# Performance work log

Measured on AMD Instinct MI355X. Metric: run time of the kernel, lower is better.

Reference implementation:

```python
import jax, jax.numpy as jnp
import numpy as np

MEMORY_SIZE = 512
PATTERN_DIM = 256
NUM_WAVELENGTHS = 3
ATTENTION_FOCUS = 1.0
CORRELATION_THRESHOLD = 0.3
H_NOISE = 0.03  # noise scale for the holographic medium buffer


def setup_inputs() -> dict:
    key = jax.random.key(0)
    k1, k2, k3 = jax.random.split(key, 3)
    B, R = 32, 128  # batch, rows per stimulus (R * PATTERN_DIM flat features)
    stimulus = jax.random.normal(k1, (B, R * PATTERN_DIM), dtype=jnp.float32)
    H_real = jax.random.normal(k2, (MEMORY_SIZE, PATTERN_DIM, NUM_WAVELENGTHS), dtype=jnp.float32) * H_NOISE
    H_imag = jax.random.normal(k3, (MEMORY_SIZE, PATTERN_DIM, NUM_WAVELENGTHS), dtype=jnp.float32) * H_NOISE
    return {"stimulus": stimulus, "H_real": H_real, "H_imag": H_imag}


def reference(stimulus, H_real, H_imag):
    # Faithful 'retrieve' mode of HolographicAssociativeMemory, fully vectorized.
    B = stimulus.shape[0]
    q = stimulus.reshape(B, -1, PATTERN_DIM).astype(jnp.complex64)  # [B, R, P]
    qf = jnp.fft.fft2(q, axes=(-2, -1))                             # [B, R, P]
    R = qf.shape[1]

    # query_fft[b, mem_idx % R] for every memory slot -> gather rows
    rows = jnp.arange(MEMORY_SIZE) % R
    q_rows = qf[:, rows, :]                                         # [B, M, P]

    H = (H_real + 1j * H_imag).astype(jnp.complex64)                # [M, P, W]
    phases = jnp.linspace(0.0, 2.0 * np.pi, NUM_WAVELENGTHS).astype(jnp.float32)
    ref_beams = jnp.exp(1j * phases).astype(jnp.complex64)          # [W]

    # reconstruction = query_fft_row * stored_hologram * reference_beam
    recon = q_rows[:, :, :, None] * H[None, :, :, :] * ref_beams    # [B, M, P, W]
    # torch.fft.ifft2 on a (1, P) tensor == ifft along P (size-1 axis is identity)
    rec = jnp.fft.ifft(recon, axis=2)                               # [B, M, P, W]
    corr = jnp.abs(rec).mean(axis=2)                                # [B, M, W]
    avg_corr = corr.mean(axis=-1)                                   # [B, M]

    focused = avg_corr * jnp.float32(ATTENTION_FOCUS)
    retrieved = jnp.where(focused > jnp.float32(CORRELATION_THRESHOLD), focused, jnp.float32(0.0))
    return retrieved
```

## Files before the change

### kernel.cpp

```cpp
#include <hip/hip_runtime.h>
#include <math.h>


#define TWO_PI 6.28318530717958647692f
#define PI_F   3.14159265358979323846f

#if __has_builtin(__builtin_amdgcn_permlane16_swap)
#define USE_PL16 1
#else
#define USE_PL16 0
#endif
#if __has_builtin(__builtin_amdgcn_permlane32_swap)
#define USE_PL32 1
#else
#define USE_PL32 0
#endif

typedef float f2 __attribute__((ext_vector_type(2)));
typedef unsigned int uint2v __attribute__((ext_vector_type(2)));

__device__ inline f2 mkf2(float x, float y) { f2 r; r[0] = x; r[1] = y; return r; }
__device__ inline f2 conjf2(f2 a) { return mkf2(a[0], -a[1]); }

__device__ inline f2 cmul(f2 a, f2 b) {
    const f2 axx = __builtin_shufflevector(a, a, 0, 0);
    const f2 ayn = mkf2(-a[1], a[1]);
    const f2 byx = __builtin_shufflevector(b, b, 1, 0);
    return axx * b + ayn * byx;
}
__device__ inline f2 csq(f2 a) { return cmul(a, a); }
__device__ inline f2 ab2(f2 A, f2 v, f2 B, f2 o) {
    const f2 Axx = __builtin_shufflevector(A, A, 0, 0);
    const f2 Ayn = mkf2(-A[1], A[1]);
    const f2 Bxx = __builtin_shufflevector(B, B, 0, 0);
    const f2 Byn = mkf2(-B[1], B[1]);
    const f2 vyx = __builtin_shufflevector(v, v, 1, 0);
    const f2 oyx = __builtin_shufflevector(o, o, 1, 0);
    return Axx * v + Ayn * vyx + Bxx * o + Byn * oyx;
}
__device__ inline f2 cfma2(f2 S, f2 b, f2 a) {
    const f2 Sxx = __builtin_shufflevector(S, S, 0, 0);
    const f2 Syn = mkf2(-S[1], S[1]);
    const f2 byx = __builtin_shufflevector(b, b, 1, 0);
    return Sxx * b + (Syn * byx + a);
}
__device__ inline f2 shfl_xor_c(f2 v, int mask) {
    return mkf2(__shfl_xor(v[0], mask, 64), __shfl_xor(v[1], mask, 64));
}

#define DPP_XOR1 0xB1
#define DPP_XOR2 0x4E
template <int CTRL>
__device__ inline f2 dpp_quad(f2 v) {
    return mkf2(
        __int_as_float(__builtin_amdgcn_update_dpp(__float_as_int(v[0]), __float_as_int(v[0]),
                                                   CTRL, 0xF, 0xF, false)),
        __int_as_float(__builtin_amdgcn_update_dpp(__float_as_int(v[1]), __float_as_int(v[1]),
                                                   CTRL, 0xF, 0xF, false)));
}

#if USE_PL16
__device__ inline void swap16c(f2 v, f2& a, f2& b) {
    uint2v rx = __builtin_amdgcn_permlane16_swap(__float_as_uint(v[0]), __float_as_uint(v[0]), false, false);
    uint2v ry = __builtin_amdgcn_permlane16_swap(__float_as_uint(v[1]), __float_as_uint(v[1]), false, false);
    a = mkf2(__uint_as_float(rx[0]), __uint_as_float(ry[0]));
    b = mkf2(__uint_as_float(rx[1]), __uint_as_float(ry[1]));
}
#endif
#if USE_PL32
__device__ inline void swap32c(f2 v, f2& a, f2& b) {
    uint2v rx = __builtin_amdgcn_permlane32_swap(__float_as_uint(v[0]), __float_as_uint(v[0]), false, false);
    uint2v ry = __builtin_amdgcn_permlane32_swap(__float_as_uint(v[1]), __float_as_uint(v[1]), false, false);
    a = mkf2(__uint_as_float(rx[0]), __uint_as_float(ry[0]));
    b = mkf2(__uint_as_float(rx[1]), __uint_as_float(ry[1]));
}
#endif

__global__ __launch_bounds__(256) void k_cols(const float* __restrict__ x,
                                              f2* __restrict__ yc,
                                              const float* __restrict__ Hr,
                                              const float* __restrict__ Hi,
                                              f2* __restrict__ Ht) {
    if (blockIdx.x >= 512) {
        const int idx = (blockIdx.x - 512) * 256 + threadIdx.x;
        const int m = idx / 768;
        const int rem = idx - m * 768;
        const int w = rem >> 8;
        const int p = rem & 255;
        const int k = __brev((unsigned)p) >> 24;
        const int src = (m * 256 + k) * 3 + w;
        Ht[idx] = mkf2(Hr[src], Hi[src]);
        return;
    }

    __shared__ f2 sm[128][17];
    __shared__ f2 tw[64];
    const int tid = threadIdx.x;

    if (tid < 64) {
        float sn, cs;
        __sincosf(-TWO_PI * (float)tid * (1.0f / 128.0f), &sn, &cs);
        tw[tid] = mkf2(cs, sn);
    }

    const int b  = blockIdx.x >> 4;
    const int d0 = (blockIdx.x & 15) << 4;
    const int c  = tid & 15;
    const int r0 = tid >> 4;
    const size_t base = (size_t)b * 32768 + (size_t)d0 + (size_t)c;

#pragma unroll
    for (int r = r0; r < 128; r += 16) {
        sm[__brev((unsigned)r) >> 25][c] = mkf2(x[base + (size_t)r * 256], 0.0f);
    }
    __syncthreads();

#pragma unroll
    for (int st = 0; st < 7; ++st) {
        const int half = 1 << st;
#pragma unroll
        for (int k = 0; k < 4; ++k) {
            const int idx = tid + (k << 8);
            const int cc  = idx & 15;
            const int j   = idx >> 4;
            const int pos = j & (half - 1);
            const int i0  = (j << 1) - pos;
            const int i1  = i0 + half;
            const f2 w  = tw[pos << (6 - st)];
            const f2 a  = sm[i0][cc];
            const f2 bv = cmul(sm[i1][cc], w);
            sm[i0][cc] = a + bv;
            sm[i1][cc] = a - bv;
        }
        __syncthreads();
    }

#pragma unroll
    for (int r = r0; r < 128; r += 16) {
        yc[base + (size_t)r * 256] = sm[r][c];
    }
}

__global__ __launch_bounds__(256) void k_recon(const f2* __restrict__ yc,
                                               const f2* __restrict__ Ht,
                                               float* __restrict__ out) {
    __shared__ f2 sh[256];
    const int lane = threadIdx.x & 63;
    const int wid  = threadIdx.x >> 6;
    const int b    = blockIdx.x >> 7;
    const int r    = blockIdx.x & 127;
    const int m    = r + (wid << 7);

    float sn, cs;
    __sincosf(PI_F * (float)lane * (1.0f / 128.0f), &sn, &cs);
    const f2 wi0 = mkf2(cs, sn);
    const f2 w64 = csq(wi0);
    const f2 S32 = csq(w64);
    const f2 S16 = csq(S32);
    const f2 b16 = csq(S16);
    const f2 b32 = csq(b16);
    const f2 b64 = csq(b32);
    const f2 one = mkf2(1.0f, 0.0f);
    const f2 A8 = (lane & 8) ? b16 : one, B8 = (lane & 8) ? one : b16;
    const f2 A4 = (lane & 4) ? b32 : one, B4 = (lane & 4) ? one : b32;
    const f2 A2 = (lane & 2) ? b64 : one, B2 = (lane & 2) ? one : b64;
    const f2 sg1 = (lane & 1) ? mkf2(-1.0f, -1.0f) : mkf2(1.0f, 1.0f);
    const f2 wi1 = mkf2(-wi0[1], wi0[0]);
#if !USE_PL16
    const f2 A16 = (lane & 16) ? S16 : one, B16 = (lane & 16) ? one : S16;
#endif
#if !USE_PL32
    const f2 A32 = (lane & 32) ? S32 : one, B32 = (lane & 32) ? one : S32;
#endif

    {
        const f2 gam    = conjf2(wi0);
        const f2 w128_0 = gam;
        const f2 w128_1 = mkf2(gam[1], -gam[0]);
        const f2 w64f = conjf2(w64);
        const f2 g4   = conjf2(S32);
        const f2 g8   = conjf2(S16);
        const f2 g16  = conjf2(b16);
        const f2 g32  = conjf2(b32);
        const f2 g64  = conjf2(b64);
#if USE_PL32
        const f2 P32 = (lane & 32) ? mkf2(-g4[0], -g4[1]) : one;
        const f2 Q32 = (lane & 32) ? g4 : one;
#else
        const f2 A32f = (lane & 32) ? g4 : one;
        const f2 B32f = (lane & 32) ? mkf2(-g4[0], -g4[1]) : one;
#endif
#if USE_PL16
        const f2 P16 = (lane & 16) ? mkf2(-g8[0], -g8[1]) : one;
        const f2 Q16 = (lane & 16) ? g8 : one;
#else
        const f2 A16f = (lane & 16) ? g8 : one;
        const f2 B16f = (lane & 16) ? mkf2(-g8[0], -g8[1]) : one;
#endif
        const f2 A8f = (lane & 8) ? g16 : one;
        const f2 B8f = (lane & 8) ? mkf2(-g16[0], -g16[1]) : one;
        const f2 A4f = (lane & 4) ? g32 : one;
        const f2 B4f = (lane & 4) ? mkf2(-g32[0], -g32[1]) : one;
        const f2 A2f = (lane & 2) ? g64 : one;
        const f2 B2f = (lane & 2) ? mkf2(-g64[0], -g64[1]) : one;

        const f2* xr = yc + ((size_t)(b * 128 + r)) * 256;
        f2 v0 = xr[lane];
        f2 v1 = xr[64 + lane];
        f2 v2 = xr[128 + lane];
        f2 v3 = xr[192 + lane];

        { f2 a = v0; v0 = a + v2; v2 = cmul(a - v2, w128_0); }
        { f2 a = v1; v1 = a + v3; v3 = cmul(a - v3, w128_1); }
        { f2 a = v0; v0 = a + v1; v1 = cmul(a - v1, w64f); }
        { f2 a = v2; v2 = a + v3; v3 = cmul(a - v3, w64f); }

        f2 u = (wid == 0) ? v0 : (wid == 1) ? v1 : (wid == 2) ? v2 : v3;

        {
#if USE_PL32
            f2 a, bb; swap32c(u, a, bb);
            u = ab2(P32, a, Q32, bb);
#else
            const f2 o = shfl_xor_c(u, 32);
            u = ab2(A32f, u, B32f, o);
#endif
        }
        {
#if USE_PL16
            f2 a, bb; swap16c(u, a, bb);
            u = ab2(P16, a, Q16, bb);
#else
            const f2 o = shfl_xor_c(u, 16);
            u = ab2(A16f, u, B16f, o);
#endif
        }
        { const f2 o = shfl_xor_c(u, 8); u = ab2(A8f, u, B8f, o); }
        { const f2 o = shfl_xor_c(u, 4); u = ab2(A4f, u, B4f, o); }
        { const f2 o = dpp_quad<DPP_XOR2>(u); u = ab2(A2f, u, B2f, o); }
        { const f2 o = dpp_quad<DPP_XOR1>(u); u = sg1 * u + o; }

        sh[(wid << 6) + lane] = u;
    }
    __syncthreads();

    f2 qv[4];
#pragma unroll
    for (int j = 0; j < 4; ++j) qv[j] = sh[j * 64 + lane];

    const f2* hp = Ht + (size_t)m * 768;
    f2 v[3][4];
#pragma unroll
    for (int w = 0; w < 3; ++w)
#pragma unroll
        for (int j = 0; j < 4; ++j)
            v[w][j] = cmul(qv[j], hp[w * 256 + j * 64 + lane]);

#pragma unroll
    for (int w = 0; w < 3; ++w)
#pragma unroll
        for (int j = 0; j < 4; ++j) {
            const f2 o = dpp_quad<DPP_XOR1>(v[w][j]);
            v[w][j] = sg1 * v[w][j] + o;
        }
#pragma unroll
    for (int w = 0; w < 3; ++w)
#pragma unroll
        for (int j = 0; j < 4; ++j) {
            const f2 o = dpp_quad<DPP_XOR2>(v[w][j]);
            v[w][j] = ab2(A2, v[w][j], B2, o);
        }
#pragma unroll
    for (int w = 0; w < 3; ++w)
#pragma unroll
        for (int j = 0; j < 4; ++j) {
            const f2 o = shfl_xor_c(v[w][j], 4);
            v[w][j] = ab2(A4, v[w][j], B4, o);
        }
#pragma unroll
    for (int w = 0; w < 3; ++w)
#pragma unroll
        for (int j = 0; j < 4; ++j) {
            const f2 o = shfl_xor_c(v[w][j], 8);
            v[w][j] = ab2(A8, v[w][j], B8, o);
        }
#pragma unroll
    for (int w = 0; w < 3; ++w)
#pragma unroll
        for (int j = 0; j < 4; ++j) {
#if USE_PL16
            f2 a, bb; swap16c(v[w][j], a, bb);
            v[w][j] = cfma2(S16, bb, a);
#else
            const f2 o = shfl_xor_c(v[w][j], 16);
            v[w][j] = ab2(A16, v[w][j], B16, o);
#endif
        }
#pragma unroll
    for (int w = 0; w < 3; ++w)
#pragma unroll
        for (int j = 0; j < 4; ++j) {
#if USE_PL32
            f2 a, bb; swap32c(v[w][j], a, bb);
            v[w][j] = cfma2(S32, bb, a);
#else
            const f2 o = shfl_xor_c(v[w][j], 32);
            v[w][j] = ab2(A32, v[w][j], B32, o);
#endif
        }
#pragma unroll
    for (int w = 0; w < 3; ++w) {
        f2 tv = cmul(w64, v[w][1]);
        f2 a = v[w][0];
        v[w][0] = a + tv; v[w][1] = a - tv;
        tv = cmul(w64, v[w][3]);
        a = v[w][2];
        v[w][2] = a + tv; v[w][3] = a - tv;
        tv = cmul(wi0, v[w][2]);
        a = v[w][0];
        v[w][0] = a + tv; v[w][2] = a - tv;
        tv = cmul(wi1, v[w][3]);
        a = v[w][1];
        v[w][1] = a + tv; v[w][3] = a - tv;
    }

    float acc = 0.0f;
#pragma unroll
    for (int w = 0; w < 3; ++w)
#pragma unroll
        for (int j = 0; j < 4; ++j) {
            const f2 sq = v[w][j] * v[w][j];
            acc += __builtin_amdgcn_sqrtf(sq[0] + sq[1]);
        }

#pragma unroll
    for (int off = 32; off > 0; off >>= 1) acc += __shfl_xor(acc, off, 64);

    if (lane == 0) {
        const float focused = acc * (1.0f / (256.0f * 256.0f * 3.0f));
        out[b * 512 + m] = (focused > 0.3f) ? focused : 0.0f;
    }
}

extern "C" void kernel_launch(void* const* d_in, const int* in_sizes, int n_in,
                              void* d_out, int out_size, void* d_ws, size_t ws_size,
                              hipStream_t stream) {
    (void)in_sizes; (void)n_in; (void)out_size; (void)ws_size;
    const float* stim = (const float*)d_in[0];
    const float* Hr   = (const float*)d_in[1];
    const float* Hi   = (const float*)d_in[2];
    float* out = (float*)d_out;

    f2* yc = (f2*)d_ws;
    f2* Ht = (f2*)((char*)d_ws + (size_t)32 * 128 * 256 * sizeof(f2));

    k_cols<<<512 + 1536, 256, 0, stream>>>(stim, yc, Hr, Hi, Ht);
    k_recon<<<4096, 256, 0, stream>>>(yc, Ht, out);
}
```

Before: 40.50 us.

## Pack two real columns per complex FFT in column-pass kernel

The column FFT now packs two real input columns (d and d+128) into one complex signal, halving the number of column-FFT blocks, and separates the two spectra using conjugate symmetry at write-out. The radix-2 FFT switches from decimation-in-time to decimation-in-frequency, so the output is in bit-reversed order, and the recon kernel reads rows through a bit-reversed index. This removes half of the column FFT arithmetic and launches, at the cost of an extra shared-memory read per output and fewer blocks for occupancy.

```diff
diff --git a/kernel.cpp b/kernel.cpp
--- a/kernel.cpp
+++ b/kernel.cpp
@@ -81,8 +81,8 @@
                                               const float* __restrict__ Hr,
                                               const float* __restrict__ Hi,
                                               f2* __restrict__ Ht) {
-    if (blockIdx.x >= 512) {
-        const int idx = (blockIdx.x - 512) * 256 + threadIdx.x;
+    if (blockIdx.x >= 256) {
+        const int idx = (blockIdx.x - 256) * 256 + threadIdx.x;
         const int m = idx / 768;
         const int rem = idx - m * 768;
         const int w = rem >> 8;
@@ -103,41 +103,53 @@
         tw[tid] = mkf2(cs, sn);
     }
 
-    const int b  = blockIdx.x >> 4;
-    const int d0 = (blockIdx.x & 15) << 4;
+    const int b  = blockIdx.x >> 3;
+    const int d0 = (blockIdx.x & 7) << 4;
     const int c  = tid & 15;
     const int r0 = tid >> 4;
-    const size_t base = (size_t)b * 32768 + (size_t)d0 + (size_t)c;
+    const int d  = d0 + c;
+    const size_t xb = (size_t)b * 32768;
 
 #pragma unroll
     for (int r = r0; r < 128; r += 16) {
-        sm[__brev((unsigned)r) >> 25][c] = mkf2(x[base + (size_t)r * 256], 0.0f);
+        sm[r][c] = mkf2(x[xb + (size_t)r * 256 + d],
+                        x[xb + (size_t)r * 256 + d + 128]);
     }
     __syncthreads();
 
 #pragma unroll
     for (int st = 0; st < 7; ++st) {
-        const int half = 1 << st;
+        const int h = 64 >> st;
 #pragma unroll
         for (int k = 0; k < 4; ++k) {
             const int idx = tid + (k << 8);
             const int cc  = idx & 15;
             const int j   = idx >> 4;
-            const int pos = j & (half - 1);
+            const int pos = j & (h - 1);
             const int i0  = (j << 1) - pos;
-            const int i1  = i0 + half;
-            const f2 w  = tw[pos << (6 - st)];
+            const int i1  = i0 + h;
+            const f2 w  = tw[pos << st];
             const f2 a  = sm[i0][cc];
-            const f2 bv = cmul(sm[i1][cc], w);
+            const f2 bv = sm[i1][cc];
             sm[i0][cc] = a + bv;
-            sm[i1][cc] = a - bv;
+            sm[i1][cc] = cmul(a - bv, w);
         }
         __syncthreads();
     }
 
 #pragma unroll
-    for (int r = r0; r < 128; r += 16) {
-        yc[base + (size_t)r * 256] = sm[r][c];
+    for (int s = r0; s < 128; s += 16) {
+        const int f  = __brev((unsigned)s) >> 25;
+        const int pf = (128 - f) & 127;
+        const int ps = __brev((unsigned)pf) >> 25;
+        const f2 Zf = sm[s][c];
+        const f2 Zp = sm[ps][c];
+        const f2 sum = mkf2((Zf[0] + Zp[0]) * 0.5f, (Zf[1] - Zp[1]) * 0.5f);
+        const f2 dif = mkf2((Zf[0] - Zp[0]) * 0.5f, (Zf[1] + Zp[1]) * 0.5f);
+        const f2 Yb  = mkf2(dif[1], -dif[0]);
+        const size_t row = ((size_t)b * 128 + s) * 256;
+        yc[row + d]       = sum;
+        yc[row + d + 128] = Yb;
     }
 }
 
@@ -150,6 +162,7 @@
     const int b    = blockIdx.x >> 7;
     const int r    = blockIdx.x & 127;
     const int m    = r + (wid << 7);
+    const int rs   = __brev((unsigned)r) >> 25;
 
     float sn, cs;
     __sincosf(PI_F * (float)lane * (1.0f / 128.0f), &sn, &cs);
@@ -204,7 +217,7 @@
         const f2 A2f = (lane & 2) ? g64 : one;
         const f2 B2f = (lane & 2) ? mkf2(-g64[0], -g64[1]) : one;
 
-        const f2* xr = yc + ((size_t)(b * 128 + r)) * 256;
+        const f2* xr = yc + ((size_t)(b * 128 + rs)) * 256;
         f2 v0 = xr[lane];
         f2 v1 = xr[64 + lane];
         f2 v2 = xr[128 + lane];
@@ -354,6 +367,6 @@
     f2* yc = (f2*)d_ws;
     f2* Ht = (f2*)((char*)d_ws + (size_t)32 * 128 * 256 * sizeof(f2));
 
-    k_cols<<<512 + 1536, 256, 0, stream>>>(stim, yc, Hr, Hi, Ht);
+    k_cols<<<256 + 1536, 256, 0, stream>>>(stim, yc, Hr, Hi, Ht);
     k_recon<<<4096, 256, 0, stream>>>(yc, Ht, out);
 }
```

After: 38.72 us. 1.05x faster.
